# Kernel tuning notes

Measured on AMD Instinct MI355X. Metric: run time of the kernel, lower is better.

Reference implementation:

```python
import jax, jax.numpy as jnp
import numpy as np

B, T, D = 2, 2048, 1024
H, KVH = 16, 4
HD = D // H            # 64
HALF = HD // 2         # 32
DFF = 4096
KW = 15
EPS = 1e-6


def zcrms(x, scale):
    # zero-centred RMSNorm: (1 + scale) * x / rms(x)
    rms = jnp.sqrt(jnp.mean(jnp.square(x.astype(jnp.float32)), axis=-1, keepdims=True) + EPS)
    return ((1.0 + scale) * x / rms).astype(x.dtype)


def apply_rope(x, cos, sin):
    # x: [B, H, T, HD]; cos/sin: [T, HALF]
    c = cos[None, None, :, :]
    s = sin[None, None, :, :]
    x1, x2 = x[..., :HALF], x[..., HALF:]
    return jnp.concatenate([x1 * c - x2 * s, x2 * c + x1 * s], axis=-1)


def setup_inputs() -> dict:
    key = jax.random.key(0)
    ks = jax.random.split(key, 20)
    std = 0.02
    inp = {
        "x": jax.random.normal(ks[0], (B, T, D), jnp.float32),
        "mask": jnp.ones((1, 1, T, T), dtype=bool),
        "cos": jnp.cos(jnp.arange(T, dtype=jnp.float32)[:, None]
                       * (10000.0 ** (-jnp.arange(HALF, dtype=jnp.float32) / HALF))[None, :]),
        "sin": jnp.sin(jnp.arange(T, dtype=jnp.float32)[:, None]
                       * (10000.0 ** (-jnp.arange(HALF, dtype=jnp.float32) / HALF))[None, :]),
        # attention
        "attn_norm_scale": jax.random.normal(ks[1], (D,), jnp.float32) * std,
        "q_kernel": jax.random.normal(ks[2], (D, D), jnp.float32) * std,
        "k_kernel": jax.random.normal(ks[3], (D, KVH * HD), jnp.float32) * std,
        "v_kernel": jax.random.normal(ks[4], (D, KVH * HD), jnp.float32) * std,
        "q_norm_scale": jax.random.normal(ks[5], (HD,), jnp.float32) * std,
        "k_norm_scale": jax.random.normal(ks[6], (HD,), jnp.float32) * std,
        "o_kernel": jax.random.normal(ks[7], (D, D), jnp.float32) * std,
        # conv module
        "conv_norm_scale": jax.random.normal(ks[8], (D,), jnp.float32) * std,
        "pw_up_kernel": jax.random.normal(ks[9], (D, 2 * D), jnp.float32) * std,
        "dw_kernel": jax.random.normal(ks[10], (KW, 1, D), jnp.float32) * std,
        "conv_inner_norm_scale": jax.random.normal(ks[11], (D,), jnp.float32) * std,
        "pw_down_kernel": jax.random.normal(ks[12], (D, D), jnp.float32) * std,
        # ffn
        "ffn_norm_scale": jax.random.normal(ks[13], (D,), jnp.float32) * std,
        "gate_kernel": jax.random.normal(ks[14], (D, DFF), jnp.float32) * std,
        "up_kernel": jax.random.normal(ks[15], (D, DFF), jnp.float32) * std,
        "down_kernel": jax.random.normal(ks[16], (DFF, D), jnp.float32) * std,
    }
    return inp


def reference(x, mask, cos, sin, attn_norm_scale, q_kernel, k_kernel, v_kernel,
              q_norm_scale, k_norm_scale, o_kernel, conv_norm_scale, pw_up_kernel,
              dw_kernel, conv_inner_norm_scale, pw_down_kernel, ffn_norm_scale,
              gate_kernel, up_kernel, down_kernel):
    # ---- pre-norm self-attention (GQA + QK-RMSNorm + RoPE) ----
    h = zcrms(x, attn_norm_scale)
    q = (h @ q_kernel).reshape(B, T, H, HD).transpose(0, 2, 1, 3)      # [B,H,T,HD]
    k = (h @ k_kernel).reshape(B, T, KVH, HD).transpose(0, 2, 1, 3)    # [B,KVH,T,HD]
    v = (h @ v_kernel).reshape(B, T, KVH, HD).transpose(0, 2, 1, 3)
    q = zcrms(q, q_norm_scale)
    k = zcrms(k, k_norm_scale)
    rep = H // KVH
    k = jnp.repeat(k, rep, axis=1)
    v = jnp.repeat(v, rep, axis=1)
    q = apply_rope(q, cos, sin)
    k = apply_rope(k, cos, sin)
    scale = jnp.sqrt(jnp.float32(HD))
    aw = jnp.einsum('bhqd,bhkd->bhqk', q, k) / scale
    aw = jnp.where(mask, aw, jnp.finfo(aw.dtype).min)
    aw = jax.nn.softmax(aw, axis=-1)
    attn = jnp.einsum('bhqk,bhkd->bhqd', aw, v).transpose(0, 2, 1, 3).reshape(B, T, D)
    x = x + attn @ o_kernel

    # ---- conformer conv module: pw_up -> GLU -> depthwise conv -> norm -> pw_down ----
    h = zcrms(x, conv_norm_scale)
    u = h @ pw_up_kernel
    u1, u2 = jnp.split(u, 2, axis=-1)
    g = u1 * jax.nn.sigmoid(u2)                                        # [B,T,D]
    c = jax.lax.conv_general_dilated(
        g, dw_kernel, window_strides=(1,), padding='SAME',
        feature_group_count=D, dimension_numbers=('NWC', 'WIO', 'NWC'))
    c = zcrms(c, conv_inner_norm_scale)
    x = x + c @ pw_down_kernel

    # ---- gated FFN with drelu activation ----
    h = zcrms(x, ffn_norm_scale)
    ff = jax.nn.relu(h @ gate_kernel) * jax.nn.relu(h @ up_kernel)
    x = x + ff @ down_kernel
    return x
```

## Files before the change

### kernel.cpp

```cpp
#include <hip/hip_runtime.h>


#define TT   2048
#define NTOK 4096

typedef __attribute__((ext_vector_type(8))) short short8;
typedef __attribute__((ext_vector_type(4))) float floatx4;

__device__ __forceinline__ unsigned short f2bf(float f) {
  unsigned int u = __float_as_uint(f);
  u = (u + 0x7fffu + ((u >> 16) & 1u)) >> 16;
  return (unsigned short)u;
}
__device__ __forceinline__ float bf2f(unsigned short s) {
  return __uint_as_float(((unsigned int)s) << 16);
}

__device__ __forceinline__ void glds16(const void* g, void* lds_base) {
  __builtin_amdgcn_global_load_lds(
      (const __attribute__((address_space(1))) void*)g,
      (__attribute__((address_space(3))) void*)lds_base, 16, 0, 0);
}

struct WJobs {
  const float* src[9];
  unsigned short* dst[9];
  int K[9], M[9], pm[9];
  int start[10];
};

__global__ __launch_bounds__(256) void wconv_all_kernel(WJobs tab) {
  int b = blockIdx.x;
  int j = 0;
  while (b >= tab.start[j + 1]) j++;
  int t = b - tab.start[j];
  const float* src = tab.src[j];
  unsigned short* dst = tab.dst[j];
  int K = tab.K[j], M = tab.M[j], pm = tab.pm[j];
  int mt = M >> 5;
  int m0 = (t % mt) * 32, k0 = (t / mt) * 32;
  int rowbase;
  if (pm == 0)      rowbase = m0;
  else if (pm == 1) rowbase = ((m0 & 1023) >> 5) * 64 + (m0 >> 10) * 32;
  else if (pm == 2) rowbase = (m0 >> 5) * 64;
  else              rowbase = (m0 >> 5) * 64 + 32;
  __shared__ float tile[32][33];
  int tx = threadIdx.x & 31, ty = threadIdx.x >> 5;
  for (int r = ty; r < 32; r += 8)
    tile[r][tx] = src[(size_t)(k0 + r) * M + m0 + tx];
  __syncthreads();
  for (int r = ty; r < 32; r += 8)
    dst[(size_t)(rowbase + r) * K + k0 + tx] = f2bf(tile[tx][r]);
}

template <bool BF16IN>
__global__ __launch_bounds__(256) void rmsnorm_kernel(
    const void* __restrict__ xin, const float* __restrict__ scale,
    unsigned short* __restrict__ out) {
  int t = blockIdx.x, tid = threadIdx.x;
  float xv[4];
  if (BF16IN) {
    ushort4 u = ((const ushort4*)((const unsigned short*)xin + (size_t)t * 1024))[tid];
    xv[0] = bf2f(u.x); xv[1] = bf2f(u.y); xv[2] = bf2f(u.z); xv[3] = bf2f(u.w);
  } else {
    float4 u = ((const float4*)((const float*)xin + (size_t)t * 1024))[tid];
    xv[0] = u.x; xv[1] = u.y; xv[2] = u.z; xv[3] = u.w;
  }
  float ss = xv[0] * xv[0] + xv[1] * xv[1] + xv[2] * xv[2] + xv[3] * xv[3];
#pragma unroll
  for (int off = 32; off > 0; off >>= 1) ss += __shfl_down(ss, off);
  __shared__ float red[4];
  if ((tid & 63) == 0) red[tid >> 6] = ss;
  __syncthreads();
  float rinv = rsqrtf((red[0] + red[1] + red[2] + red[3]) * (1.0f / 1024.0f) + 1e-6f);
  float4 sv = ((const float4*)scale)[tid];
  ushort4 o;
  o.x = f2bf((1.0f + sv.x) * xv[0] * rinv);
  o.y = f2bf((1.0f + sv.y) * xv[1] * rinv);
  o.z = f2bf((1.0f + sv.z) * xv[2] * rinv);
  o.w = f2bf((1.0f + sv.w) * xv[3] * rinv);
  ((ushort4*)(out + (size_t)t * 1024))[tid] = o;
}

template <int BN, int FUSE, int OUT, int RES>
__device__ __forceinline__ void gemm_body(
    const unsigned short* __restrict__ A, const unsigned short* __restrict__ Bt,
    void* __restrict__ Cout, const void* __restrict__ resid, int K, int M) {
  constexpr int NI = BN / 32;
  __shared__ __align__(16) unsigned short As[128 * 64];
  __shared__ __align__(16) unsigned short Bs[BN * 64];
  const int tid = threadIdx.x;
  const int wid = tid >> 6, lane = tid & 63;
  const int quad = lane >> 4, l16 = lane & 15;
  const int wm = (wid >> 1) * 64, wn = (wid & 1) * (BN / 2);

  int bx = blockIdx.x, by = blockIdx.y;
  if ((gridDim.x & 7) == 0) {
    int pid = by * gridDim.x + bx;
    int inb = pid & 63, pidp = pid >> 6;
    by = (pidp & 3) * 8 + (inb & 7);
    bx = (pidp >> 2) * 8 + (inb >> 3);
  }
  const int row0 = by * 128;
  const int col0 = bx * BN;

  floatx4 acc[4][NI];
#pragma unroll
  for (int mi = 0; mi < 4; mi++)
#pragma unroll
    for (int ni = 0; ni < NI; ni++) acc[mi][ni] = (floatx4){0.f, 0.f, 0.f, 0.f};

  const unsigned short* Ag = A + (size_t)row0 * K;
  const unsigned short* Bg = Bt + (size_t)col0 * K;

  for (int k0 = 0; k0 < K; k0 += 64) {
#pragma unroll
    for (int j = 0; j < 4; j++) {
      int ci = tid + j * 256;
      int r = ci >> 3, c = (ci & 7) ^ (r & 7);
      glds16(Ag + (size_t)r * K + k0 + c * 8, &As[(wid * 64 + j * 256) * 8]);
    }
#pragma unroll
    for (int j = 0; j < BN / 32; j++) {
      int ci = tid + j * 256;
      int r = ci >> 3, c = (ci & 7) ^ (r & 7);
      glds16(Bg + (size_t)r * K + k0 + c * 8, &Bs[(wid * 64 + j * 256) * 8]);
    }
    __syncthreads();
#pragma unroll
    for (int kk = 0; kk < 64; kk += 32) {
      short8 a[4], b[NI];
#pragma unroll
      for (int mi = 0; mi < 4; mi++) {
        int r = wm + mi * 16 + l16;
        a[mi] = *(const short8*)&As[r * 64 + (((kk >> 3) + quad) ^ (r & 7)) * 8];
      }
#pragma unroll
      for (int ni = 0; ni < NI; ni++) {
        int r = wn + ni * 16 + l16;
        b[ni] = *(const short8*)&Bs[r * 64 + (((kk >> 3) + quad) ^ (r & 7)) * 8];
      }
#pragma unroll
      for (int mi = 0; mi < 4; mi++)
#pragma unroll
        for (int ni = 0; ni < NI; ni++)
          acc[mi][ni] = __builtin_amdgcn_mfma_f32_16x16x32_bf16(a[mi], b[ni], acc[mi][ni], 0, 0, 0);
    }
    __syncthreads();
  }

  if (FUSE == 0) {
#pragma unroll
    for (int mi = 0; mi < 4; mi++) {
#pragma unroll
      for (int reg = 0; reg < 4; reg++) {
        int grow = row0 + wm + mi * 16 + quad * 4 + reg;
#pragma unroll
        for (int ni = 0; ni < NI; ni++) {
          int gcol = col0 + wn + ni * 16 + l16;
          float v = acc[mi][ni][reg];
          if (RES == 1) v += ((const float*)resid)[(size_t)grow * M + gcol];
          if (RES == 2) v += bf2f(((const unsigned short*)resid)[(size_t)grow * M + gcol]);
          if (OUT == 1) ((unsigned short*)Cout)[(size_t)grow * M + gcol] = f2bf(v);
          else          ((float*)Cout)[(size_t)grow * M + gcol] = v;
        }
      }
    }
  } else {
    const int group = (col0 + wn) >> 6;
    const int MW = M >> 1;
#pragma unroll
    for (int mi = 0; mi < 4; mi++) {
#pragma unroll
      for (int reg = 0; reg < 4; reg++) {
        int grow = row0 + wm + mi * 16 + quad * 4 + reg;
#pragma unroll
        for (int ni = 0; ni < NI / 2; ni++) {
          int f = group * 32 + ni * 16 + l16;
          float a = acc[mi][ni][reg], b = acc[mi][ni + NI / 2][reg];
          float v;
          if (FUSE == 1) v = a / (1.0f + __expf(-b));
          else           v = fmaxf(a, 0.f) * fmaxf(b, 0.f);
          ((unsigned short*)Cout)[(size_t)grow * MW + f] = f2bf(v);
        }
      }
    }
  }
}

__global__ __launch_bounds__(256, 2) void gemm_qkv(
    const unsigned short* A, const unsigned short* Bt, void* C, const void* r, int K, int M) {
  gemm_body<128, 0, 1, 0>(A, Bt, C, r, K, M);
}
__global__ __launch_bounds__(256, 2) void gemm_oproj(
    const unsigned short* A, const unsigned short* Bt, void* C, const void* r, int K, int M) {
  gemm_body<64, 0, 1, 1>(A, Bt, C, r, K, M);
}
__global__ __launch_bounds__(256, 2) void gemm_glu(
    const unsigned short* A, const unsigned short* Bt, void* C, const void* r, int K, int M) {
  gemm_body<128, 1, 1, 0>(A, Bt, C, r, K, M);
}
__global__ __launch_bounds__(256, 2) void gemm_dn(
    const unsigned short* A, const unsigned short* Bt, void* C, const void* r, int K, int M) {
  gemm_body<64, 0, 1, 2>(A, Bt, C, r, K, M);
}
__global__ __launch_bounds__(256, 2) void gemm_gateup(
    const unsigned short* A, const unsigned short* Bt, void* C, const void* r, int K, int M) {
  gemm_body<128, 2, 1, 0>(A, Bt, C, r, K, M);
}
__global__ __launch_bounds__(256, 2) void gemm_ffdn(
    const unsigned short* A, const unsigned short* Bt, void* C, const void* r, int K, int M) {
  gemm_body<64, 0, 0, 2>(A, Bt, C, r, K, M);
}

#define QSCALE 0.180336880111f

__global__ __launch_bounds__(256) void qknorm_rope_kernel(
    const unsigned short* __restrict__ qkv, const float* __restrict__ cosb,
    const float* __restrict__ sinb, const float* __restrict__ qns,
    const float* __restrict__ kns, unsigned short* __restrict__ qb,
    unsigned short* __restrict__ kb) {
  int tok = blockIdx.x;
  int tid = threadIdx.x, w = tid >> 6, lane = tid & 63;
  int pos = tok & (TT - 1);
  int half = lane & 31;
  float c = cosb[pos * 32 + half], s = sinb[pos * 32 + half];
  const unsigned short* row = qkv + (size_t)tok * 1536;
  for (int hr = w; hr < 20; hr += 4) {
    float v = bf2f(row[hr * 64 + lane]);
    float ss = v * v;
#pragma unroll
    for (int off = 32; off > 0; off >>= 1) ss += __shfl_xor(ss, off);
    float rinv = rsqrtf(ss * (1.0f / 64.0f) + 1e-6f);
    float sc = (hr < 16) ? qns[lane] : kns[lane];
    float nv = (1.0f + sc) * v * rinv;
    float partner = __shfl_xor(nv, 32);
    float outv = (lane < 32) ? (nv * c - partner * s) : (nv * c + partner * s);
    if (hr < 16) qb[(size_t)tok * 1024 + hr * 64 + lane] = f2bf(outv * QSCALE);
    else         kb[(size_t)tok * 256 + (hr - 16) * 64 + lane] = f2bf(outv);
  }
}

__global__ __launch_bounds__(256) void vtrans_kernel(
    const unsigned short* __restrict__ qkv, unsigned short* __restrict__ vt) {
  __shared__ unsigned short t[64 * 65];
  int ktile = blockIdx.x;
  int g = blockIdx.y;
  int bi = g >> 2, kvh = g & 3;
  int tid = threadIdx.x;
#pragma unroll
  for (int j = 0; j < 2; j++) {
    int ci = tid + j * 256;
    int r = ci >> 3, c8 = (ci & 7) * 8;
    union { uint4 v; unsigned short u[8]; } uu;
    uu.v = *(const uint4*)(qkv + (size_t)(bi * TT + ktile * 64 + r) * 1536 +
                           1280 + kvh * 64 + c8);
#pragma unroll
    for (int e = 0; e < 8; e++) t[r * 65 + c8 + e] = uu.u[e];
  }
  __syncthreads();
#pragma unroll
  for (int j = 0; j < 2; j++) {
    int ci = tid + j * 256;
    int d = ci >> 3, c8 = (ci & 7) * 8;
    union { uint4 v; unsigned short u[8]; } uu;
#pragma unroll
    for (int e = 0; e < 8; e++) uu.u[e] = t[(c8 + e) * 65 + d];
    *(uint4*)(vt + ((size_t)(g * 64 + d)) * TT + ktile * 64 + c8) = uu.v;
  }
}

__global__ __launch_bounds__(512) void flash_kernel(
    const unsigned short* __restrict__ qb, const unsigned short* __restrict__ kb,
    const unsigned short* __restrict__ vt, unsigned short* __restrict__ ob) {
  const int qt = blockIdx.x;
  const int bh = blockIdx.y;
  const int bi = bh >> 4, h = bh & 15, kvh = h >> 2;
  const int tid = threadIdx.x, w = tid >> 6, lane = tid & 63;
  const int quad = lane >> 4, l16 = lane & 15;

  __shared__ __align__(16) unsigned short Ks[2][64 * 64];
  __shared__ __align__(16) unsigned short Vs[2][64 * 64];
  __shared__ __align__(16) unsigned short Ps[256 * 64];

  const unsigned short* qsrc = qb + ((size_t)(bi * TT + qt * 256)) * 1024 + h * 64;
  short8 qf[2][2];
#pragma unroll
  for (int af = 0; af < 2; af++) {
    const unsigned short* qr = qsrc + (size_t)(w * 32 + af * 16 + l16) * 1024;
    qf[af][0] = *(const short8*)(qr + quad * 8);
    qf[af][1] = *(const short8*)(qr + 32 + quad * 8);
  }

  const unsigned short* kbase = kb + ((size_t)(bi * TT)) * 256 + kvh * 64;
  const unsigned short* vbase = vt + ((size_t)(bi * 4 + kvh)) * (64 * TT);

  floatx4 oacc[2][4];
  floatx4 lacc[2];
#pragma unroll
  for (int af = 0; af < 2; af++) {
    lacc[af] = (floatx4){0.f, 0.f, 0.f, 0.f};
#pragma unroll
    for (int di = 0; di < 4; di++) oacc[af][di] = (floatx4){0.f, 0.f, 0.f, 0.f};
  }
  const short8 ones = (short8){0x3F80, 0x3F80, 0x3F80, 0x3F80,
                               0x3F80, 0x3F80, 0x3F80, 0x3F80};

  {
    int r = tid >> 3, c = (tid & 7) ^ (r & 7);
    glds16(kbase + (size_t)r * 256 + c * 8, &Ks[0][w * 512]);
    glds16(vbase + (size_t)r * TT + c * 8, &Vs[0][w * 512]);
  }

  for (int kt = 0; kt < 32; kt++) {
    const int buf = kt & 1;
    __syncthreads();
    if (kt < 31) {
      int r = tid >> 3, c = (tid & 7) ^ (r & 7);
      glds16(kbase + (size_t)((kt + 1) * 64 + r) * 256 + c * 8, &Ks[buf ^ 1][w * 512]);
      glds16(vbase + (size_t)r * TT + (kt + 1) * 64 + c * 8, &Vs[buf ^ 1][w * 512]);
    }

    short8 kf[4][2];
#pragma unroll
    for (int ni = 0; ni < 4; ni++) {
      int rb = ni * 16 + l16;
      kf[ni][0] = *(const short8*)&Ks[buf][rb * 64 + ((quad ^ (rb & 7)) * 8)];
      kf[ni][1] = *(const short8*)&Ks[buf][rb * 64 + (((4 + quad) ^ (rb & 7)) * 8)];
    }
#pragma unroll
    for (int af = 0; af < 2; af++) {
      const int rr = w * 32 + af * 16 + l16;
#pragma unroll
      for (int ni = 0; ni < 4; ni++) {
        floatx4 s = (floatx4){0.f, 0.f, 0.f, 0.f};
        s = __builtin_amdgcn_mfma_f32_16x16x32_bf16(kf[ni][0], qf[af][0], s, 0, 0, 0);
        s = __builtin_amdgcn_mfma_f32_16x16x32_bf16(kf[ni][1], qf[af][1], s, 0, 0, 0);
        union { unsigned short u[4]; unsigned long long ull; } pk;
#pragma unroll
        for (int r = 0; r < 4; r++)
          pk.u[r] = (unsigned short)(__float_as_uint(__builtin_amdgcn_exp2f(s[r])) >> 16);
        int ch = (ni * 2 + (quad >> 1)) ^ (rr & 7);
        *(unsigned long long*)&Ps[rr * 64 + ch * 8 + (quad & 1) * 4] = pk.ull;
      }
    }
    short8 vf[4][2];
#pragma unroll
    for (int di = 0; di < 4; di++) {
      int rb = di * 16 + l16;
      vf[di][0] = *(const short8*)&Vs[buf][rb * 64 + ((quad ^ (rb & 7)) * 8)];
      vf[di][1] = *(const short8*)&Vs[buf][rb * 64 + (((4 + quad) ^ (rb & 7)) * 8)];
    }
#pragma unroll
    for (int af = 0; af < 2; af++) {
      const int rr = w * 32 + af * 16 + l16;
      short8 pa0 = *(const short8*)&Ps[rr * 64 + ((quad ^ (rr & 7)) * 8)];
      short8 pa1 = *(const short8*)&Ps[rr * 64 + (((4 + quad) ^ (rr & 7)) * 8)];
      lacc[af] = __builtin_amdgcn_mfma_f32_16x16x32_bf16(pa0, ones, lacc[af], 0, 0, 0);
      lacc[af] = __builtin_amdgcn_mfma_f32_16x16x32_bf16(pa1, ones, lacc[af], 0, 0, 0);
#pragma unroll
      for (int di = 0; di < 4; di++) {
        oacc[af][di] = __builtin_amdgcn_mfma_f32_16x16x32_bf16(pa0, vf[di][0], oacc[af][di], 0, 0, 0);
        oacc[af][di] = __builtin_amdgcn_mfma_f32_16x16x32_bf16(pa1, vf[di][1], oacc[af][di], 0, 0, 0);
      }
    }
  }

  unsigned short* obase = ob + ((size_t)(bi * TT + qt * 256)) * 1024 + h * 64;
#pragma unroll
  for (int af = 0; af < 2; af++) {
    float rl[4];
#pragma unroll
    for (int r = 0; r < 4; r++) rl[r] = 1.0f / lacc[af][r];
#pragma unroll
    for (int di = 0; di < 4; di++)
#pragma unroll
      for (int r = 0; r < 4; r++) {
        int qrow = w * 32 + af * 16 + quad * 4 + r;
        obase[(size_t)qrow * 1024 + di * 16 + l16] = f2bf(oacc[af][di][r] * rl[r]);
      }
  }
}

__global__ __launch_bounds__(256) void convnorm_kernel(
    const unsigned short* __restrict__ g, const float* __restrict__ dw,
    const float* __restrict__ scale, unsigned short* __restrict__ out) {
  int tok = blockIdx.x;
  int bi = tok >> 11, pos = tok & (TT - 1);
  int tid = threadIdx.x, c0 = tid * 4;
  float a0 = 0.f, a1 = 0.f, a2 = 0.f, a3 = 0.f;
#pragma unroll
  for (int wk = 0; wk < 15; wk++) {
    int pp = pos + wk - 7;
    if (pp < 0 || pp >= TT) continue;
    ushort4 gv = *(const ushort4*)(g + ((size_t)(bi * TT + pp)) * 1024 + c0);
    float4 kv = *(const float4*)(dw + wk * 1024 + c0);
    a0 += bf2f(gv.x) * kv.x;
    a1 += bf2f(gv.y) * kv.y;
    a2 += bf2f(gv.z) * kv.z;
    a3 += bf2f(gv.w) * kv.w;
  }
  float ss = a0 * a0 + a1 * a1 + a2 * a2 + a3 * a3;
#pragma unroll
  for (int off = 32; off > 0; off >>= 1) ss += __shfl_down(ss, off);
  __shared__ float red[4];
  if ((tid & 63) == 0) red[tid >> 6] = ss;
  __syncthreads();
  float rinv = rsqrtf((red[0] + red[1] + red[2] + red[3]) * (1.0f / 1024.0f) + 1e-6f);
  float4 sv = *(const float4*)(scale + c0);
  ushort4 o;
  o.x = f2bf((1.0f + sv.x) * a0 * rinv);
  o.y = f2bf((1.0f + sv.y) * a1 * rinv);
  o.z = f2bf((1.0f + sv.z) * a2 * rinv);
  o.w = f2bf((1.0f + sv.w) * a3 * rinv);
  *(ushort4*)(out + (size_t)tok * 1024 + c0) = o;
}

extern "C" void kernel_launch(void* const* d_in, const int* in_sizes, int n_in,
                              void* d_out, int out_size, void* d_ws, size_t ws_size,
                              hipStream_t stream) {
  const float* x        = (const float*)d_in[0];
  const float* cosb     = (const float*)d_in[2];
  const float* sinb     = (const float*)d_in[3];
  const float* attn_ns  = (const float*)d_in[4];
  const float* qkern    = (const float*)d_in[5];
  const float* kkern    = (const float*)d_in[6];
  const float* vkern    = (const float*)d_in[7];
  const float* qns      = (const float*)d_in[8];
  const float* kns      = (const float*)d_in[9];
  const float* okern    = (const float*)d_in[10];
  const float* conv_ns  = (const float*)d_in[11];
  const float* pwupk    = (const float*)d_in[12];
  const float* dwk      = (const float*)d_in[13];
  const float* convi_ns = (const float*)d_in[14];
  const float* pwdnk    = (const float*)d_in[15];
  const float* ffn_ns   = (const float*)d_in[16];
  const float* gatek    = (const float*)d_in[17];
  const float* upk      = (const float*)d_in[18];
  const float* downk    = (const float*)d_in[19];
  float* out = (float*)d_out;
  char* ws = (char*)d_ws;

  const size_t O_QKVT = 0;
  const size_t O_OT   = O_QKVT + (size_t)1536 * 1024 * 2;
  const size_t O_UPT  = O_OT   + (size_t)1024 * 1024 * 2;
  const size_t O_DNT  = O_UPT  + (size_t)2048 * 1024 * 2;
  const size_t O_GUT  = O_DNT  + (size_t)1024 * 1024 * 2;
  const size_t O_DWNT = O_GUT  + (size_t)8192 * 1024 * 2;
  const size_t O_H    = O_DWNT + (size_t)4096 * 1024 * 2;
  const size_t O_BIG1 = O_H    + (size_t)4096 * 1024 * 2;
  const size_t O_QB   = O_BIG1 + (size_t)4096 * 8192 * 2;
  const size_t O_KB   = O_QB   + (size_t)4096 * 1024 * 2;
  const size_t O_VT   = O_KB   + (size_t)4096 * 256 * 2;
  const size_t O_ECN  = O_VT   + (size_t)8 * 64 * 2048 * 2;
  const size_t O_X1   = O_ECN  + (size_t)4096 * 1024 * 2;
  const size_t O_X2   = O_X1   + (size_t)4096 * 1024 * 2;
  const size_t O_BIG2 = O_X2   + (size_t)4096 * 1024 * 2;

  unsigned short* qkvT = (unsigned short*)(ws + O_QKVT);
  unsigned short* oT   = (unsigned short*)(ws + O_OT);
  unsigned short* upT  = (unsigned short*)(ws + O_UPT);
  unsigned short* dnT  = (unsigned short*)(ws + O_DNT);
  unsigned short* guT  = (unsigned short*)(ws + O_GUT);
  unsigned short* dwT  = (unsigned short*)(ws + O_DWNT);
  unsigned short* hbuf = (unsigned short*)(ws + O_H);
  unsigned short* big1u = (unsigned short*)(ws + O_BIG1);
  unsigned short* qbuf = (unsigned short*)(ws + O_QB);
  unsigned short* kbuf = (unsigned short*)(ws + O_KB);
  unsigned short* vtb  = (unsigned short*)(ws + O_VT);
  unsigned short* ecn  = (unsigned short*)(ws + O_ECN);
  unsigned short* x1b  = (unsigned short*)(ws + O_X1);
  unsigned short* x2b  = (unsigned short*)(ws + O_X2);
  unsigned short* big2 = (unsigned short*)(ws + O_BIG2);

  WJobs tab;
  tab.src[0] = qkern;  tab.dst[0] = qkvT;                       tab.K[0] = 1024; tab.M[0] = 1024; tab.pm[0] = 0;
  tab.src[1] = kkern;  tab.dst[1] = qkvT + (size_t)1024 * 1024; tab.K[1] = 1024; tab.M[1] = 256;  tab.pm[1] = 0;
  tab.src[2] = vkern;  tab.dst[2] = qkvT + (size_t)1280 * 1024; tab.K[2] = 1024; tab.M[2] = 256;  tab.pm[2] = 0;
  tab.src[3] = okern;  tab.dst[3] = oT;                         tab.K[3] = 1024; tab.M[3] = 1024; tab.pm[3] = 0;
  tab.src[4] = pwupk;  tab.dst[4] = upT;                        tab.K[4] = 1024; tab.M[4] = 2048; tab.pm[4] = 1;
  tab.src[5] = pwdnk;  tab.dst[5] = dnT;                        tab.K[5] = 1024; tab.M[5] = 1024; tab.pm[5] = 0;
  tab.src[6] = gatek;  tab.dst[6] = guT;                        tab.K[6] = 1024; tab.M[6] = 4096; tab.pm[6] = 2;
  tab.src[7] = upk;    tab.dst[7] = guT;                        tab.K[7] = 1024; tab.M[7] = 4096; tab.pm[7] = 3;
  tab.src[8] = downk;  tab.dst[8] = dwT;                        tab.K[8] = 4096; tab.M[8] = 1024; tab.pm[8] = 0;
  tab.start[0] = 0;
  for (int i = 0; i < 9; i++)
    tab.start[i + 1] = tab.start[i] + (tab.M[i] >> 5) * (tab.K[i] >> 5);
  wconv_all_kernel<<<tab.start[9], 256, 0, stream>>>(tab);

  rmsnorm_kernel<false><<<NTOK, 256, 0, stream>>>(x, attn_ns, hbuf);
  gemm_qkv<<<dim3(12, 32), 256, 0, stream>>>(hbuf, qkvT, big1u, nullptr, 1024, 1536);
  qknorm_rope_kernel<<<NTOK, 256, 0, stream>>>(big1u, cosb, sinb, qns, kns,
                                               qbuf, kbuf);
  vtrans_kernel<<<dim3(32, 8), 256, 0, stream>>>(big1u, vtb);
  flash_kernel<<<dim3(8, 32), 512, 0, stream>>>(qbuf, kbuf, vtb, ecn);
  gemm_oproj<<<dim3(16, 32), 256, 0, stream>>>(ecn, oT, x1b, x, 1024, 1024);

  rmsnorm_kernel<true><<<NTOK, 256, 0, stream>>>(x1b, conv_ns, hbuf);
  gemm_glu<<<dim3(16, 32), 256, 0, stream>>>(hbuf, upT, big2, nullptr, 1024, 2048);
  convnorm_kernel<<<NTOK, 256, 0, stream>>>(big2, dwk, convi_ns, ecn);
  gemm_dn<<<dim3(16, 32), 256, 0, stream>>>(ecn, dnT, x2b, x1b, 1024, 1024);

  rmsnorm_kernel<true><<<NTOK, 256, 0, stream>>>(x2b, ffn_ns, hbuf);
  gemm_gateup<<<dim3(64, 32), 256, 0, stream>>>(hbuf, guT, big1u, nullptr, 1024, 8192);
  gemm_ffdn<<<dim3(16, 32), 256, 0, stream>>>(big1u, dwT, out, x2b, 4096, 1024);
}
```

Measured before the change: 484.8 us.

## Fuse QK norm, RoPE and V transpose into the QKV GEMM epilogue

Replaces the generic QKV GEMM plus separate qknorm/rope and V-transpose kernels with one GEMM whose epilogue does per-head RMS norm, rotary embedding, Q scaling, and writes V transposed directly. This removes two launches and the round trip of the intermediate QKV buffer through global memory. The swizzle guard changes to apply only when gridDim.x is 16, so this grid (12 wide) gets no swizzle. Epilogue stores become scattered 2-byte writes for Q/K, which could be less coalesced.

```diff
diff --git a/kernel.cpp b/kernel.cpp
--- a/kernel.cpp
+++ b/kernel.cpp
@@ -95,7 +95,7 @@
   const int wm = (wid >> 1) * 64, wn = (wid & 1) * (BN / 2);
 
   int bx = blockIdx.x, by = blockIdx.y;
-  if ((gridDim.x & 7) == 0) {
+  if (gridDim.x == 16) {
     int pid = by * gridDim.x + bx;
     int inb = pid & 63, pidp = pid >> 6;
     by = (pidp & 3) * 8 + (inb & 7);
@@ -188,10 +188,6 @@
   }
 }
 
-__global__ __launch_bounds__(256, 2) void gemm_qkv(
-    const unsigned short* A, const unsigned short* Bt, void* C, const void* r, int K, int M) {
-  gemm_body<128, 0, 1, 0>(A, Bt, C, r, K, M);
-}
 __global__ __launch_bounds__(256, 2) void gemm_oproj(
     const unsigned short* A, const unsigned short* Bt, void* C, const void* r, int K, int M) {
   gemm_body<64, 0, 1, 1>(A, Bt, C, r, K, M);
@@ -215,58 +211,115 @@
 
 #define QSCALE 0.180336880111f
 
-__global__ __launch_bounds__(256) void qknorm_rope_kernel(
-    const unsigned short* __restrict__ qkv, const float* __restrict__ cosb,
-    const float* __restrict__ sinb, const float* __restrict__ qns,
-    const float* __restrict__ kns, unsigned short* __restrict__ qb,
-    unsigned short* __restrict__ kb) {
-  int tok = blockIdx.x;
-  int tid = threadIdx.x, w = tid >> 6, lane = tid & 63;
-  int pos = tok & (TT - 1);
-  int half = lane & 31;
-  float c = cosb[pos * 32 + half], s = sinb[pos * 32 + half];
-  const unsigned short* row = qkv + (size_t)tok * 1536;
-  for (int hr = w; hr < 20; hr += 4) {
-    float v = bf2f(row[hr * 64 + lane]);
-    float ss = v * v;
-#pragma unroll
-    for (int off = 32; off > 0; off >>= 1) ss += __shfl_xor(ss, off);
-    float rinv = rsqrtf(ss * (1.0f / 64.0f) + 1e-6f);
-    float sc = (hr < 16) ? qns[lane] : kns[lane];
-    float nv = (1.0f + sc) * v * rinv;
-    float partner = __shfl_xor(nv, 32);
-    float outv = (lane < 32) ? (nv * c - partner * s) : (nv * c + partner * s);
-    if (hr < 16) qb[(size_t)tok * 1024 + hr * 64 + lane] = f2bf(outv * QSCALE);
-    else         kb[(size_t)tok * 256 + (hr - 16) * 64 + lane] = f2bf(outv);
-  }
-}
-
-__global__ __launch_bounds__(256) void vtrans_kernel(
-    const unsigned short* __restrict__ qkv, unsigned short* __restrict__ vt) {
-  __shared__ unsigned short t[64 * 65];
-  int ktile = blockIdx.x;
-  int g = blockIdx.y;
-  int bi = g >> 2, kvh = g & 3;
-  int tid = threadIdx.x;
-#pragma unroll
-  for (int j = 0; j < 2; j++) {
-    int ci = tid + j * 256;
-    int r = ci >> 3, c8 = (ci & 7) * 8;
-    union { uint4 v; unsigned short u[8]; } uu;
-    uu.v = *(const uint4*)(qkv + (size_t)(bi * TT + ktile * 64 + r) * 1536 +
-                           1280 + kvh * 64 + c8);
-#pragma unroll
-    for (int e = 0; e < 8; e++) t[r * 65 + c8 + e] = uu.u[e];
-  }
-  __syncthreads();
-#pragma unroll
-  for (int j = 0; j < 2; j++) {
-    int ci = tid + j * 256;
-    int d = ci >> 3, c8 = (ci & 7) * 8;
-    union { uint4 v; unsigned short u[8]; } uu;
-#pragma unroll
-    for (int e = 0; e < 8; e++) uu.u[e] = t[(c8 + e) * 65 + d];
-    *(uint4*)(vt + ((size_t)(g * 64 + d)) * TT + ktile * 64 + c8) = uu.v;
+__global__ __launch_bounds__(256, 2) void gemm_qkvf(
+    const unsigned short* __restrict__ A, const unsigned short* __restrict__ Bt,
+    const float* __restrict__ cosb, const float* __restrict__ sinb,
+    const float* __restrict__ qns, const float* __restrict__ kns,
+    unsigned short* __restrict__ qb, unsigned short* __restrict__ kb,
+    unsigned short* __restrict__ vt) {
+  constexpr int K = 1024;
+  __shared__ __align__(16) unsigned short As[128 * 64];
+  __shared__ __align__(16) unsigned short Bs[128 * 64];
+  const int tid = threadIdx.x;
+  const int wid = tid >> 6, lane = tid & 63;
+  const int quad = lane >> 4, l16 = lane & 15;
+  const int wm = (wid >> 1) * 64, wn = (wid & 1) * 64;
+  const int row0 = blockIdx.y * 128;
+  const int col0 = blockIdx.x * 128;
+
+  floatx4 acc[4][4];
+#pragma unroll
+  for (int mi = 0; mi < 4; mi++)
+#pragma unroll
+    for (int ni = 0; ni < 4; ni++) acc[mi][ni] = (floatx4){0.f, 0.f, 0.f, 0.f};
+
+  const unsigned short* Ag = A + (size_t)row0 * K;
+  const unsigned short* Bg = Bt + (size_t)col0 * K;
+
+  for (int k0 = 0; k0 < K; k0 += 64) {
+#pragma unroll
+    for (int j = 0; j < 4; j++) {
+      int ci = tid + j * 256;
+      int r = ci >> 3, c = (ci & 7) ^ (r & 7);
+      glds16(Ag + (size_t)r * K + k0 + c * 8, &As[(wid * 64 + j * 256) * 8]);
+      glds16(Bg + (size_t)r * K + k0 + c * 8, &Bs[(wid * 64 + j * 256) * 8]);
+    }
+    __syncthreads();
+#pragma unroll
+    for (int kk = 0; kk < 64; kk += 32) {
+      short8 a[4], b[4];
+#pragma unroll
+      for (int mi = 0; mi < 4; mi++) {
+        int r = wm + mi * 16 + l16;
+        a[mi] = *(const short8*)&As[r * 64 + (((kk >> 3) + quad) ^ (r & 7)) * 8];
+      }
+#pragma unroll
+      for (int ni = 0; ni < 4; ni++) {
+        int r = wn + ni * 16 + l16;
+        b[ni] = *(const short8*)&Bs[r * 64 + (((kk >> 3) + quad) ^ (r & 7)) * 8];
+      }
+#pragma unroll
+      for (int mi = 0; mi < 4; mi++)
+#pragma unroll
+        for (int ni = 0; ni < 4; ni++)
+          acc[mi][ni] = __builtin_amdgcn_mfma_f32_16x16x32_bf16(a[mi], b[ni], acc[mi][ni], 0, 0, 0);
+    }
+    __syncthreads();
+  }
+
+  const int head = (col0 + wn) >> 6;
+  const int bi = row0 >> 11;
+
+  if (head < 20) {
+    const float* ns = (head < 16) ? qns : kns;
+    float sc[4];
+#pragma unroll
+    for (int ni = 0; ni < 4; ni++) sc[ni] = 1.0f + ns[ni * 16 + l16];
+#pragma unroll
+    for (int mi = 0; mi < 4; mi++) {
+#pragma unroll
+      for (int reg = 0; reg < 4; reg++) {
+        int row = row0 + wm + mi * 16 + quad * 4 + reg;
+        int pos = row & (TT - 1);
+        float ss = acc[mi][0][reg] * acc[mi][0][reg] + acc[mi][1][reg] * acc[mi][1][reg] +
+                   acc[mi][2][reg] * acc[mi][2][reg] + acc[mi][3][reg] * acc[mi][3][reg];
+        ss += __shfl_xor(ss, 1); ss += __shfl_xor(ss, 2);
+        ss += __shfl_xor(ss, 4); ss += __shfl_xor(ss, 8);
+        float rinv = rsqrtf(ss * (1.0f / 64.0f) + 1e-6f);
+        float c0 = cosb[pos * 32 + l16],      s0 = sinb[pos * 32 + l16];
+        float c1 = cosb[pos * 32 + 16 + l16], s1 = sinb[pos * 32 + 16 + l16];
+        float nv0 = sc[0] * acc[mi][0][reg] * rinv;
+        float nv1 = sc[1] * acc[mi][1][reg] * rinv;
+        float nv2 = sc[2] * acc[mi][2][reg] * rinv;
+        float nv3 = sc[3] * acc[mi][3][reg] * rinv;
+        float o0 = nv0 * c0 - nv2 * s0;
+        float o1 = nv1 * c1 - nv3 * s1;
+        float o2 = nv2 * c0 + nv0 * s0;
+        float o3 = nv3 * c1 + nv1 * s1;
+        if (head < 16) {
+          unsigned short* d = qb + (size_t)row * 1024 + head * 64 + l16;
+          d[0] = f2bf(o0 * QSCALE); d[16] = f2bf(o1 * QSCALE);
+          d[32] = f2bf(o2 * QSCALE); d[48] = f2bf(o3 * QSCALE);
+        } else {
+          unsigned short* d = kb + (size_t)row * 256 + (head - 16) * 64 + l16;
+          d[0] = f2bf(o0); d[16] = f2bf(o1); d[32] = f2bf(o2); d[48] = f2bf(o3);
+        }
+      }
+    }
+  } else {
+    const int g = bi * 4 + (head - 20);
+    const int key0 = (row0 & (TT - 1)) + wm + quad * 4;
+#pragma unroll
+    for (int mi = 0; mi < 4; mi++) {
+#pragma unroll
+      for (int ni = 0; ni < 4; ni++) {
+        int d = ni * 16 + l16;
+        ushort4 pk;
+        pk.x = f2bf(acc[mi][ni][0]); pk.y = f2bf(acc[mi][ni][1]);
+        pk.z = f2bf(acc[mi][ni][2]); pk.w = f2bf(acc[mi][ni][3]);
+        *(ushort4*)(vt + ((size_t)(g * 64 + d)) * TT + key0 + mi * 16) = pk;
+      }
+    }
   }
 }
 
@@ -489,10 +542,8 @@
   wconv_all_kernel<<<tab.start[9], 256, 0, stream>>>(tab);
 
   rmsnorm_kernel<false><<<NTOK, 256, 0, stream>>>(x, attn_ns, hbuf);
-  gemm_qkv<<<dim3(12, 32), 256, 0, stream>>>(hbuf, qkvT, big1u, nullptr, 1024, 1536);
-  qknorm_rope_kernel<<<NTOK, 256, 0, stream>>>(big1u, cosb, sinb, qns, kns,
-                                               qbuf, kbuf);
-  vtrans_kernel<<<dim3(32, 8), 256, 0, stream>>>(big1u, vtb);
+  gemm_qkvf<<<dim3(12, 32), 256, 0, stream>>>(hbuf, qkvT, cosb, sinb, qns, kns,
+                                              qbuf, kbuf, vtb);
   flash_kernel<<<dim3(8, 32), 512, 0, stream>>>(qbuf, kbuf, vtb, ecn);
   gemm_oproj<<<dim3(16, 32), 256, 0, stream>>>(ecn, oT, x1b, x, 1024, 1024);
 
```

Result: faster. 457.6 us (-5.6%).
